# Kernel tuning notes

Hardware: AMD Instinct MI355X
Metric: run time of the kernel (lower is better)

The kernel has to match this reference:

```python
import jax, jax.numpy as jnp
import numpy as np

B, N, D = 4096, 128, 256


def setup_inputs() -> dict:
    key = jax.random.key(0)
    ks = jax.random.split(key, 6)
    return {
        "label": jax.random.normal(ks[0], (B, N, D), dtype=jnp.float32),
        "adj_in": jax.random.uniform(ks[1], (N, N), dtype=jnp.float32),
        "adj_out": jax.random.uniform(ks[2], (N, N), dtype=jnp.float32),
        "edge_bias": jnp.zeros((N, D), dtype=jnp.float32),
        "gate_weight": jax.random.normal(ks[3], (D, 1), dtype=jnp.float32) * (6.0 / (D + 1)) ** 0.5,
        "bias_gate": jnp.zeros((N, 1), dtype=jnp.float32),
        "out_edge_bias": jnp.zeros((N, D), dtype=jnp.float32),
        "out_gate_weight": jax.random.normal(ks[4], (D, 1), dtype=jnp.float32) * (6.0 / (D + 1)) ** 0.5,
        "out_bias_gate": jnp.zeros((N, 1), dtype=jnp.float32),
        "loop_gate": jax.random.normal(ks[5], (D, 1), dtype=jnp.float32) * (6.0 / (D + 1)) ** 0.5,
    }


def reference(label, adj_in, adj_out, edge_bias, gate_weight, bias_gate,
              out_edge_bias, out_gate_weight, out_bias_gate, loop_gate):
    h = label  # [B, N, D]
    # origin_adj is a constant buffer in the original module (detached numpy)
    origin = jax.lax.stop_gradient(jnp.where(adj_in <= 0, adj_in, 1.0))

    # in-arc branch: masked dense adjacency matmul + bias + scalar gate
    h_in = jnp.einsum('mn,bnd->bmd', origin * adj_in, h)            # [B, N, D]
    in_gate = jnp.einsum('bnd,do->bno', h, gate_weight) + bias_gate  # [B, N, 1]
    msg_in = (h_in + edge_bias) * jax.nn.sigmoid(in_gate)

    # out-arc branch: transposed mask times out adjacency
    h_out = jnp.einsum('mn,bnd->bmd', origin.T * adj_out, h)
    out_gate = jnp.einsum('bnd,do->bno', h, out_gate_weight) + out_bias_gate
    msg_out = (h_out + out_edge_bias) * jax.nn.sigmoid(out_gate)

    # self-loop branch
    lp_gate = jnp.einsum('bnd,do->bno', h, loop_gate)
    msg_loop = h * jax.nn.sigmoid(lp_gate)

    # dropout p=0.0 -> identity
    return jax.nn.relu(msg_in + msg_out + msg_loop)
```

## Files before the change

### kernel.cpp

```cpp
#include <hip/hip_runtime.h>
#include <hip/hip_bf16.h>

#define NN 128
#define ND 256

#define SWZ(d) ((((d) ^ ((d) >> 2)) & 15) << 3)

typedef __attribute__((ext_vector_type(8))) short short8v;
typedef __attribute__((ext_vector_type(4))) float floatx4;
typedef __attribute__((ext_vector_type(2))) unsigned int uint2v;
typedef __attribute__((ext_vector_type(4))) unsigned int uint4v;

__device__ __forceinline__ unsigned short f2bf(float x){
  unsigned u = __float_as_uint(x);
  u += 0x7FFF + ((u >> 16) & 1);
  return (unsigned short)(u >> 16);
}
__device__ __forceinline__ float bf2f(unsigned short h){
  return __uint_as_float(((unsigned)h) << 16);
}
__device__ __forceinline__ unsigned pk2(float a, float b){
  float2 t; t.x = a; t.y = b;
  __hip_bfloat162 hh = __float22bfloat162_rn(t);
  unsigned r;
  __builtin_memcpy(&r, &hh, 4);
  return r;
}

__global__ void prep_A(const float* __restrict__ adj_in, const float* __restrict__ adj_out,
                       const float* __restrict__ gw, const float* __restrict__ ogw,
                       const float* __restrict__ lw, unsigned short* __restrict__ Abf){
  int idx = blockIdx.x * 256 + threadIdx.x;
  if (idx < 32768){
    int m = idx >> 7, n = idx & 127;
    float v;
    if (m < NN){
      float a = adj_in[m * NN + n];
      v = (a <= 0.f) ? a * a : a;
    } else {
      int mm = m - NN;
      float t = adj_in[n * NN + mm];
      float o = (t <= 0.f) ? t : 1.f;
      v = o * adj_out[mm * NN + n];
    }
    Abf[idx] = f2bf(v);
  } else if (idx < 32768 + 4096){
    int t   = idx - 32768;
    int j   = t & 7, m16 = (t >> 3) & 15, g = (t >> 7) & 3, kc = t >> 9;
    int d   = kc * 32 + 8 * g + j;
    float v = (m16 == 0) ? gw[d] : (m16 == 1) ? ogw[d] : (m16 == 2) ? lw[d] : 0.f;
    Abf[idx] = f2bf(v);
  }
}

__global__ __launch_bounds__(512, 4) void gcn_main(
    const float* __restrict__ H, const unsigned short* __restrict__ Abf,
    const float* __restrict__ eb,  const float* __restrict__ bg,
    const float* __restrict__ oeb, const float* __restrict__ obg,
    float* __restrict__ Out)
{
  __shared__ __align__(16) unsigned short Ht[ND * NN];
  __shared__ float sigS[3 * NN];

  const int tid  = threadIdx.x;
  const int wave = tid >> 6;
  const int lane = tid & 63;
  const int g    = lane >> 4;
  const int m16  = lane & 15;
  const int b    = (blockIdx.x & 7) * 512 + (blockIdx.x >> 3);
  const float* Hb = H   + (size_t)b * NN * ND;
  float*       Ob = Out + (size_t)b * NN * ND;
  const unsigned short* WgT = Abf + 32768;

  const int n0   = 4 * (4 * wave + g);
  const int arow = 16 * wave + m16;

  floatx4 gacc = {0.f, 0.f, 0.f, 0.f};
  #pragma unroll
  for (int s = 0; s < 2; ++s){
    const int ds0 = 128 * s;
    floatx4 rr[2][4];
    #pragma unroll
    for (int dq = 0; dq < 2; ++dq)
      #pragma unroll
      for (int ro = 0; ro < 4; ++ro)
        rr[dq][ro] = *(const floatx4*)(Hb + (size_t)(n0 + ro) * ND + ds0 + 64 * dq + 4 * m16);
    #pragma unroll
    for (int t = 0; t < 4; ++t){
      const int k0 = ds0 + 32 * t;
      const short8v wv = *(const short8v*)&WgT[(((k0 >> 5) * 4 + g) * 16 + m16) * 8];
      const floatx4 f0 = *(const floatx4*)(Hb + (size_t)arow * ND + k0 + 8 * g);
      const floatx4 f1 = *(const floatx4*)(Hb + (size_t)arow * ND + k0 + 8 * g + 4);
      uint4v au;
      au[0] = pk2(f0[0], f0[1]); au[1] = pk2(f0[2], f0[3]);
      au[2] = pk2(f1[0], f1[1]); au[3] = pk2(f1[2], f1[3]);
      short8v af;
      __builtin_memcpy(&af, &au, 16);
      gacc = __builtin_amdgcn_mfma_f32_16x16x32_bf16(af, wv, gacc, 0, 0, 0);
    }
    #pragma unroll
    for (int dq = 0; dq < 2; ++dq){
      #pragma unroll
      for (int j = 0; j < 4; ++j){
        const int d = ds0 + 64 * dq + 4 * m16 + j;
        uint2v pv;
        pv[0] = pk2(rr[dq][0][j], rr[dq][1][j]);
        pv[1] = pk2(rr[dq][2][j], rr[dq][3][j]);
        *(uint2v*)&Ht[d * NN + (n0 ^ SWZ(d))] = pv;
      }
    }
  }
  if (m16 < 3){
    #pragma unroll
    for (int r = 0; r < 4; ++r){
      const int n = 16 * wave + 4 * g + r;
      float x = gacc[r];
      if (m16 == 0)      x += bg[n];
      else if (m16 == 1) x += obg[n];
      sigS[m16 * NN + n] = 1.f / (1.f + __expf(-x));
    }
  }
  __syncthreads();

  const float si = sigS[arow];
  const float so = sigS[NN + arow];
  const float sl = sigS[2 * NN + arow];

  #pragma unroll
  for (int p = 0; p < 4; ++p){
    floatx4 ebv[4], oebv[4];
    #pragma unroll
    for (int df2 = 0; df2 < 4; ++df2){
      const int dcol = 16 * (4 * p + df2) + 4 * g;
      ebv[df2]  = *(const floatx4*)(eb  + arow * ND + dcol);
      oebv[df2] = *(const floatx4*)(oeb + arow * ND + dcol);
    }

    floatx4 acc1[4], acc2[4];
    #pragma unroll
    for (int i = 0; i < 4; ++i){
      acc1[i] = (floatx4){0.f,0.f,0.f,0.f};
      acc2[i] = (floatx4){0.f,0.f,0.f,0.f};
    }
    __builtin_amdgcn_s_setprio(1);
    #pragma unroll
    for (int k0 = 0; k0 < 128; k0 += 32){
      const int kk = k0 + 8 * g;
      const short8v av1 = *(const short8v*)&Abf[ arow        * 128 + kk];
      const short8v av2 = *(const short8v*)&Abf[(128 + arow) * 128 + kk];
      #pragma unroll
      for (int df2 = 0; df2 < 4; ++df2){
        const int d = 16 * (4 * p + df2) + m16;
        const short8v hv = *(const short8v*)&Ht[d * NN + (kk ^ SWZ(d))];
        acc1[df2] = __builtin_amdgcn_mfma_f32_16x16x32_bf16(hv, av1, acc1[df2], 0, 0, 0);
        acc2[df2] = __builtin_amdgcn_mfma_f32_16x16x32_bf16(hv, av2, acc2[df2], 0, 0, 0);
      }
    }
    __builtin_amdgcn_s_setprio(0);

    #pragma unroll
    for (int df2 = 0; df2 < 4; ++df2){
      const int dcol = 16 * (4 * p + df2) + 4 * g;
      floatx4 o;
      #pragma unroll
      for (int r = 0; r < 4; ++r){
        const int d = dcol + r;
        const float hl = bf2f(Ht[d * NN + (arow ^ SWZ(d))]);
        const float v = (acc1[df2][r] + ebv[df2][r]) * si
                      + (acc2[df2][r] + oebv[df2][r]) * so
                      + hl * sl;
        o[r] = fmaxf(v, 0.f);
      }
      *(floatx4*)(Ob + (size_t)arow * ND + dcol) = o;
    }
  }
}

extern "C" void kernel_launch(void* const* d_in, const int* in_sizes, int n_in,
                              void* d_out, int out_size, void* d_ws, size_t ws_size,
                              hipStream_t stream){
  const float* H    = (const float*)d_in[0];
  const float* ain  = (const float*)d_in[1];
  const float* aout = (const float*)d_in[2];
  const float* eb   = (const float*)d_in[3];
  const float* gwp  = (const float*)d_in[4];
  const float* bgp  = (const float*)d_in[5];
  const float* oebp = (const float*)d_in[6];
  const float* ogwp = (const float*)d_in[7];
  const float* obgp = (const float*)d_in[8];
  const float* lwp  = (const float*)d_in[9];
  unsigned short* Abf = (unsigned short*)d_ws;

  prep_A<<<144, 256, 0, stream>>>(ain, aout, gwp, ogwp, lwp, Abf);
  gcn_main<<<4096, 512, 0, stream>>>(H, Abf, eb, bgp, oebp, obgp, (float*)d_out);
}
```

Measured before the change: 409.2 us.

## Halve LDS tile by staging H in two D-halves to raise occupancy

The transposed bf16 H tile in shared memory is cut from 256x128 to 128x128 elements. The kernel now computes the gate GEMV over all of D first, stages one half of D, processes it, then syncs and restages the second half. Launch bounds go from 4 to 6 blocks per CU to take advantage of the smaller LDS footprint. The cost is an extra pair of barriers and less overlap between global loads and MFMA work, and the second half's H load is serialized after the first half's compute. Edge-bias loads were also moved into the epilogue to cut register pressure.

```diff
diff --git a/kernel.cpp b/kernel.cpp
--- a/kernel.cpp
+++ b/kernel.cpp
@@ -53,13 +53,13 @@
   }
 }
 
-__global__ __launch_bounds__(512, 4) void gcn_main(
+__global__ __launch_bounds__(512, 6) void gcn_main(
     const float* __restrict__ H, const unsigned short* __restrict__ Abf,
     const float* __restrict__ eb,  const float* __restrict__ bg,
     const float* __restrict__ oeb, const float* __restrict__ obg,
     float* __restrict__ Out)
 {
-  __shared__ __align__(16) unsigned short Ht[ND * NN];
+  __shared__ __align__(16) unsigned short Ht[128 * NN];
   __shared__ float sigS[3 * NN];
 
   const int tid  = threadIdx.x;
@@ -75,41 +75,41 @@
   const int n0   = 4 * (4 * wave + g);
   const int arow = 16 * wave + m16;
 
-  floatx4 gacc = {0.f, 0.f, 0.f, 0.f};
-  #pragma unroll
-  for (int s = 0; s < 2; ++s){
-    const int ds0 = 128 * s;
+  auto stage_half = [&](int h){
     floatx4 rr[2][4];
     #pragma unroll
     for (int dq = 0; dq < 2; ++dq)
       #pragma unroll
       for (int ro = 0; ro < 4; ++ro)
-        rr[dq][ro] = *(const floatx4*)(Hb + (size_t)(n0 + ro) * ND + ds0 + 64 * dq + 4 * m16);
-    #pragma unroll
-    for (int t = 0; t < 4; ++t){
-      const int k0 = ds0 + 32 * t;
-      const short8v wv = *(const short8v*)&WgT[(((k0 >> 5) * 4 + g) * 16 + m16) * 8];
-      const floatx4 f0 = *(const floatx4*)(Hb + (size_t)arow * ND + k0 + 8 * g);
-      const floatx4 f1 = *(const floatx4*)(Hb + (size_t)arow * ND + k0 + 8 * g + 4);
-      uint4v au;
-      au[0] = pk2(f0[0], f0[1]); au[1] = pk2(f0[2], f0[3]);
-      au[2] = pk2(f1[0], f1[1]); au[3] = pk2(f1[2], f1[3]);
-      short8v af;
-      __builtin_memcpy(&af, &au, 16);
-      gacc = __builtin_amdgcn_mfma_f32_16x16x32_bf16(af, wv, gacc, 0, 0, 0);
-    }
+        rr[dq][ro] = *(const floatx4*)(Hb + (size_t)(n0 + ro) * ND + 128 * h + 64 * dq + 4 * m16);
     #pragma unroll
     for (int dq = 0; dq < 2; ++dq){
       #pragma unroll
       for (int j = 0; j < 4; ++j){
-        const int d = ds0 + 64 * dq + 4 * m16 + j;
+        const int d = 64 * dq + 4 * m16 + j;
         uint2v pv;
         pv[0] = pk2(rr[dq][0][j], rr[dq][1][j]);
         pv[1] = pk2(rr[dq][2][j], rr[dq][3][j]);
         *(uint2v*)&Ht[d * NN + (n0 ^ SWZ(d))] = pv;
       }
     }
+  };
+
+  floatx4 gacc = {0.f, 0.f, 0.f, 0.f};
+  #pragma unroll
+  for (int c = 0; c < 8; ++c){
+    const int k0 = 32 * c;
+    const short8v wv = *(const short8v*)&WgT[((c * 4 + g) * 16 + m16) * 8];
+    const floatx4 f0 = *(const floatx4*)(Hb + (size_t)arow * ND + k0 + 8 * g);
+    const floatx4 f1 = *(const floatx4*)(Hb + (size_t)arow * ND + k0 + 8 * g + 4);
+    uint4v au;
+    au[0] = pk2(f0[0], f0[1]); au[1] = pk2(f0[2], f0[3]);
+    au[2] = pk2(f1[0], f1[1]); au[3] = pk2(f1[2], f1[3]);
+    short8v af;
+    __builtin_memcpy(&af, &au, 16);
+    gacc = __builtin_amdgcn_mfma_f32_16x16x32_bf16(af, wv, gacc, 0, 0, 0);
   }
+  stage_half(0);
   if (m16 < 3){
     #pragma unroll
     for (int r = 0; r < 4; ++r){
@@ -127,51 +127,54 @@
   const float sl = sigS[2 * NN + arow];
 
   #pragma unroll
-  for (int p = 0; p < 4; ++p){
-    floatx4 ebv[4], oebv[4];
+  for (int h = 0; h < 2; ++h){
+    if (h == 1){
+      __syncthreads();
+      stage_half(1);
+      __syncthreads();
+    }
     #pragma unroll
-    for (int df2 = 0; df2 < 4; ++df2){
-      const int dcol = 16 * (4 * p + df2) + 4 * g;
-      ebv[df2]  = *(const floatx4*)(eb  + arow * ND + dcol);
-      oebv[df2] = *(const floatx4*)(oeb + arow * ND + dcol);
-    }
+    for (int p2 = 0; p2 < 2; ++p2){
+      floatx4 acc1[4], acc2[4];
+      #pragma unroll
+      for (int i = 0; i < 4; ++i){
+        acc1[i] = (floatx4){0.f,0.f,0.f,0.f};
+        acc2[i] = (floatx4){0.f,0.f,0.f,0.f};
+      }
+      __builtin_amdgcn_s_setprio(1);
+      #pragma unroll
+      for (int k0 = 0; k0 < 128; k0 += 32){
+        const int kk = k0 + 8 * g;
+        const short8v av1 = *(const short8v*)&Abf[ arow        * 128 + kk];
+        const short8v av2 = *(const short8v*)&Abf[(128 + arow) * 128 + kk];
+        #pragma unroll
+        for (int df2 = 0; df2 < 4; ++df2){
+          const int d = 16 * (4 * p2 + df2) + m16;
+          const short8v hv = *(const short8v*)&Ht[d * NN + (kk ^ SWZ(d))];
+          acc1[df2] = __builtin_amdgcn_mfma_f32_16x16x32_bf16(hv, av1, acc1[df2], 0, 0, 0);
+          acc2[df2] = __builtin_amdgcn_mfma_f32_16x16x32_bf16(hv, av2, acc2[df2], 0, 0, 0);
+        }
+      }
+      __builtin_amdgcn_s_setprio(0);
 
-    floatx4 acc1[4], acc2[4];
-    #pragma unroll
-    for (int i = 0; i < 4; ++i){
-      acc1[i] = (floatx4){0.f,0.f,0.f,0.f};
-      acc2[i] = (floatx4){0.f,0.f,0.f,0.f};
-    }
-    __builtin_amdgcn_s_setprio(1);
-    #pragma unroll
-    for (int k0 = 0; k0 < 128; k0 += 32){
-      const int kk = k0 + 8 * g;
-      const short8v av1 = *(const short8v*)&Abf[ arow        * 128 + kk];
-      const short8v av2 = *(const short8v*)&Abf[(128 + arow) * 128 + kk];
       #pragma unroll
       for (int df2 = 0; df2 < 4; ++df2){
-        const int d = 16 * (4 * p + df2) + m16;
-        const short8v hv = *(const short8v*)&Ht[d * NN + (kk ^ SWZ(d))];
-        acc1[df2] = __builtin_amdgcn_mfma_f32_16x16x32_bf16(hv, av1, acc1[df2], 0, 0, 0);
-        acc2[df2] = __builtin_amdgcn_mfma_f32_16x16x32_bf16(hv, av2, acc2[df2], 0, 0, 0);
+        const int dloc = 16 * (4 * p2 + df2) + 4 * g;
+        const int dglob = 128 * h + dloc;
+        const floatx4 ebv  = *(const floatx4*)(eb  + arow * ND + dglob);
+        const floatx4 oebv = *(const floatx4*)(oeb + arow * ND + dglob);
+        floatx4 o;
+        #pragma unroll
+        for (int r = 0; r < 4; ++r){
+          const int d = dloc + r;
+          const float hl = bf2f(Ht[d * NN + (arow ^ SWZ(d))]);
+          const float v = (acc1[df2][r] + ebv[r]) * si
+                        + (acc2[df2][r] + oebv[r]) * so
+                        + hl * sl;
+          o[r] = fmaxf(v, 0.f);
+        }
+        *(floatx4*)(Ob + (size_t)arow * ND + dglob) = o;
       }
-    }
-    __builtin_amdgcn_s_setprio(0);
-
-    #pragma unroll
-    for (int df2 = 0; df2 < 4; ++df2){
-      const int dcol = 16 * (4 * p + df2) + 4 * g;
-      floatx4 o;
-      #pragma unroll
-      for (int r = 0; r < 4; ++r){
-        const int d = dcol + r;
-        const float hl = bf2f(Ht[d * NN + (arow ^ SWZ(d))]);
-        const float v = (acc1[df2][r] + ebv[df2][r]) * si
-                      + (acc2[df2][r] + oebv[df2][r]) * so
-                      + hl * sl;
-        o[r] = fmaxf(v, 0.f);
-      }
-      *(floatx4*)(Ob + (size_t)arow * ND + dcol) = o;
     }
   }
 }
```

Result: slower. 617.6 us (+50.9%).
